# Optimization experiments

Hardware: AMD Instinct MI355X
Metric: run time of the kernel (lower is better)

## Reference

```python
import jax, jax.numpy as jnp
import numpy as np

NUM_CAPS = 10        # num_output_capsules
OUT_CH = 16          # output_cap_channels (output capsule dim)
IN_CH = 256
H = W = 6
PRIM_DIM = 8
NUM_PRIM = OUT_CH * H * W // PRIM_DIM  # 72 primary capsule vectors per branch
NUM_ITERS = 3
EPS = 1e-8


def squash(s, axis=-1):
    # v = (|s|^2 / (1 + |s|^2)) * s / |s|
    sq = jnp.sum(s * s, axis=axis, keepdims=True)
    return (sq / (1.0 + sq)) * s * jax.lax.rsqrt(sq + EPS)


def setup_inputs() -> dict:
    key = jax.random.key(0)
    k1, k2, k3, k4 = jax.random.split(key, 4)
    B = 2048
    x = jax.random.normal(k1, (B, IN_CH, H, W), dtype=jnp.float32)
    # per-output-capsule 1x1 conv: weight [K, out_ch, in_ch], bias [K, out_ch]
    conv_w = jax.random.normal(k2, (NUM_CAPS, OUT_CH, IN_CH), dtype=jnp.float32) * (1.0 / np.sqrt(IN_CH))
    conv_b = jnp.zeros((NUM_CAPS, OUT_CH), dtype=jnp.float32)
    # transformation matrices: [K, P, prim_dim, out_dim]
    weights = jax.random.normal(k3, (NUM_CAPS, NUM_PRIM, PRIM_DIM, OUT_CH), dtype=jnp.float32)
    return {"x": x, "conv_w": conv_w, "conv_b": conv_b, "weights": weights}


def reference(x, conv_w, conv_b, weights):
    B = x.shape[0]
    # 1x1 conv per output capsule branch: [B, K, out_ch, H, W]
    caps = jnp.einsum('bchw,koc->bkohw', x, conv_w) + conv_b[None, :, :, None, None]
    # flatten + reshape into primary capsule vectors: [B, K, P, 8]
    prim = caps.reshape(B, NUM_CAPS, NUM_PRIM, PRIM_DIM)
    # prediction vectors u = prim @ W : [B, K, P, 16]
    u = jnp.einsum('bkpd,kpde->bkpe', prim, weights)
    # dynamic routing by agreement
    b = jnp.zeros((B, NUM_CAPS, NUM_PRIM), dtype=u.dtype)
    v = None
    for _ in range(NUM_ITERS):
        c = jax.nn.softmax(b, axis=1)                 # coupling over output capsules
        s = jnp.einsum('bkp,bkpe->bke', c, u)         # weighted sum over primaries
        v = squash(s, axis=-1)                        # [B, K, 16]
        b = b + jnp.einsum('bkpe,bke->bkp', u, v)     # agreement
    return v
```

## Files before the change

### kernel.cpp

```cpp
#include <hip/hip_runtime.h>
#include <stdint.h>

#define KCAPS 10
#define OC    16
#define IC    256
#define HWSZ  36
#define PRIM  72
#define PD    8
#define EDIM  16
#define BMAX  2048

typedef short bf16x8 __attribute__((ext_vector_type(8)));
typedef float f32x4  __attribute__((ext_vector_type(4)));

__device__ unsigned short g_whi[KCAPS * OC * IC];
__device__ unsigned short g_wlo[KCAPS * OC * IC];
__device__ float4         g_wtsT4[KCAPS * PD * 4 * PRIM];
__device__ float          g_caps_fallback[(size_t)BMAX * 160 * HWSZ];

#define SMEM_G 76032
#define SMEM_B (13194 * 4)

__device__ __forceinline__ void bf_split(float v, unsigned short& hb, unsigned short& lb) {
    __bf16 h = (__bf16)v;
    hb = __builtin_bit_cast(unsigned short, h);
    __bf16 l = (__bf16)(v - (float)h);
    lb = __builtin_bit_cast(unsigned short, l);
}

__device__ __forceinline__ f32x4 mfma16(bf16x8 a, bf16x8 b, f32x4 c) {
    return __builtin_amdgcn_mfma_f32_16x16x32_bf16(a, b, c, 0, 0, 0);
}

__global__ __launch_bounds__(256)
void prep_kernel(const float* __restrict__ w, const float* __restrict__ wts) {
    int i = blockIdx.x * 256 + threadIdx.x;
    if (i < KCAPS * OC * IC) {
        unsigned short hb, lb;
        bf_split(w[i], hb, lb);
        g_whi[i] = hb;
        g_wlo[i] = lb;
    }
    if (i < KCAPS * PD * 4 * PRIM) {
        int p = i % PRIM;
        int r = i / PRIM;
        int e4 = r & 3;
        int d  = (r >> 2) & 7;
        int k  = r >> 5;
        g_wtsT4[i] = *(const float4*)(wts + (size_t)(((k * PRIM + p) * PD + d) * EDIM + e4 * 4));
    }
}

__global__ __launch_bounds__(256, 2)
void gemm_caps(const float* __restrict__ x, const float* __restrict__ conv_b,
               float* __restrict__ caps_g) {
    extern __shared__ char smem[];
    uint32_t* xs_u = (uint32_t*)smem;
    const short* xs_s = (const short*)smem;

    const int t  = threadIdx.x;
    const int bb = blockIdx.x;
    const int wv = t >> 6;
    const int ln = t & 63;
    const int row = ln & 15;
    const int g   = ln >> 4;
    const int nm  = (wv < 2) ? 3 : 2;

    for (int task = t; task < 2304; task += 256) {
        int half = (task >= 1152) ? 1 : 0;
        int tt = task - half * 1152;
        int cp = tt / 9, hq = tt - cp * 9;
        const float4* x4 = (const float4*)(x + (size_t)(2 * bb + half) * (IC * HWSZ));
        float4 va = x4[(2 * cp) * 9 + hq];
        float4 vb = x4[(2 * cp + 1) * 9 + hq];
        uint32_t* xh = xs_u + half * 9504;
        uint32_t* xl = xh + 4752;
        int base = (4 * hq) * 132 + cp;
        unsigned short ha, la, hb, lb;
        bf_split(va.x, ha, la); bf_split(vb.x, hb, lb);
        xh[base]       = (uint32_t)ha | ((uint32_t)hb << 16);
        xl[base]       = (uint32_t)la | ((uint32_t)lb << 16);
        bf_split(va.y, ha, la); bf_split(vb.y, hb, lb);
        xh[base + 132] = (uint32_t)ha | ((uint32_t)hb << 16);
        xl[base + 132] = (uint32_t)la | ((uint32_t)lb << 16);
        bf_split(va.z, ha, la); bf_split(vb.z, hb, lb);
        xh[base + 264] = (uint32_t)ha | ((uint32_t)hb << 16);
        xl[base + 264] = (uint32_t)la | ((uint32_t)lb << 16);
        bf_split(va.w, ha, la); bf_split(vb.w, hb, lb);
        xh[base + 396] = (uint32_t)ha | ((uint32_t)hb << 16);
        xl[base + 396] = (uint32_t)la | ((uint32_t)lb << 16);
    }
    __syncthreads();

    const int hwbase[3] = {0, 16, 20};

    f32x4 acc0[3][3] = {}, acc1[3][3] = {};
    for (int kt = 0; kt < 8; ++kt) {
        bf16x8 bh[3], bl[3];
        #pragma unroll
        for (int mi = 0; mi < 3; ++mi) {
            if (mi < nm) {
                int woff = ((wv + 4 * mi) * 16 + row) * 256 + kt * 32 + g * 8;
                bh[mi] = *(const bf16x8*)(g_whi + woff);
                bl[mi] = *(const bf16x8*)(g_wlo + woff);
            }
        }
        bf16x8 ah0[3], al0[3], ah1[3], al1[3];
        #pragma unroll
        for (int nt = 0; nt < 3; ++nt) {
            int o2 = (hwbase[nt] + row) * 264 + kt * 32 + g * 8;
            ah0[nt] = *(const bf16x8*)(xs_s + o2);
            al0[nt] = *(const bf16x8*)(xs_s + 9504 + o2);
            ah1[nt] = *(const bf16x8*)(xs_s + 19008 + o2);
            al1[nt] = *(const bf16x8*)(xs_s + 28512 + o2);
        }
        #pragma unroll
        for (int mi = 0; mi < 3; ++mi) {
            if (mi < nm) {
                #pragma unroll
                for (int nt = 0; nt < 3; ++nt) {
                    acc0[mi][nt] = mfma16(ah0[nt], bh[mi], acc0[mi][nt]);
                    acc1[mi][nt] = mfma16(ah1[nt], bh[mi], acc1[mi][nt]);
                    acc0[mi][nt] = mfma16(al0[nt], bh[mi], acc0[mi][nt]);
                    acc1[mi][nt] = mfma16(al1[nt], bh[mi], acc1[mi][nt]);
                    acc0[mi][nt] = mfma16(ah0[nt], bl[mi], acc0[mi][nt]);
                    acc1[mi][nt] = mfma16(ah1[nt], bl[mi], acc1[mi][nt]);
                }
            }
        }
    }

    float* cg0 = caps_g + (size_t)(2 * bb) * (160 * HWSZ);
    float* cg1 = caps_g + (size_t)(2 * bb + 1) * (160 * HWSZ);
    #pragma unroll
    for (int mi = 0; mi < 3; ++mi) {
        if (mi < nm) {
            int m = (wv + 4 * mi) * 16 + row;
            float bias = conv_b[m];
            #pragma unroll
            for (int nt = 0; nt < 3; ++nt) {
                int hw0 = hwbase[nt] + g * 4;
                if (nt < 2 || g == 3) {
                    float4 o0, o1;
                    o0.x = acc0[mi][nt][0] + bias; o1.x = acc1[mi][nt][0] + bias;
                    o0.y = acc0[mi][nt][1] + bias; o1.y = acc1[mi][nt][1] + bias;
                    o0.z = acc0[mi][nt][2] + bias; o1.z = acc1[mi][nt][2] + bias;
                    o0.w = acc0[mi][nt][3] + bias; o1.w = acc1[mi][nt][3] + bias;
                    *(float4*)(cg0 + m * HWSZ + hw0) = o0;
                    *(float4*)(cg1 + m * HWSZ + hw0) = o1;
                }
            }
        }
    }
}

__global__ __launch_bounds__(256, 2)
void route_kernel(const float* __restrict__ caps_g, float* __restrict__ out) {
    extern __shared__ char smem[];
    float* u_t     = (float*)smem;
    float* b_s     = u_t + 16 * 724;
    float* c_s     = b_s + 720;
    float* v_s     = c_s + 720;
    float* scale_s = v_s + 160;

    const int t  = threadIdx.x;
    const int bb = blockIdx.x;

    {
        const float4* cg4 = (const float4*)(caps_g + (size_t)bb * (160 * HWSZ));
        for (int task = t; task < KCAPS * PRIM; task += 256) {
            int k = task / PRIM;
            int p = task - k * PRIM;
            float4 c0 = cg4[task * 2];
            float4 c1 = cg4[task * 2 + 1];
            float pv[PD] = {c0.x, c0.y, c0.z, c0.w, c1.x, c1.y, c1.z, c1.w};
            const float4* wb = g_wtsT4 + k * (PD * 4 * PRIM) + p;
            float au[EDIM] = {};
            #pragma unroll
            for (int d = 0; d < PD; ++d) {
                #pragma unroll
                for (int e4 = 0; e4 < 4; ++e4) {
                    float4 w4 = wb[(d * 4 + e4) * PRIM];
                    au[e4 * 4 + 0] = fmaf(pv[d], w4.x, au[e4 * 4 + 0]);
                    au[e4 * 4 + 1] = fmaf(pv[d], w4.y, au[e4 * 4 + 1]);
                    au[e4 * 4 + 2] = fmaf(pv[d], w4.z, au[e4 * 4 + 2]);
                    au[e4 * 4 + 3] = fmaf(pv[d], w4.w, au[e4 * 4 + 3]);
                }
            }
            #pragma unroll
            for (int e = 0; e < EDIM; ++e) u_t[e * 724 + task] = au[e];
        }
    }
    for (int i = t; i < KCAPS * PRIM; i += 256) b_s[i] = 0.f;
    __syncthreads();

    for (int it = 0; it < 3; ++it) {
        if (t < PRIM) {
            float bv[KCAPS];
            float m = -1e30f;
            #pragma unroll
            for (int k2 = 0; k2 < KCAPS; ++k2) { bv[k2] = b_s[k2 * PRIM + t]; m = fmaxf(m, bv[k2]); }
            float sum = 0.f;
            #pragma unroll
            for (int k2 = 0; k2 < KCAPS; ++k2) { bv[k2] = __expf(bv[k2] - m); sum += bv[k2]; }
            float inv = 1.f / sum;
            #pragma unroll
            for (int k2 = 0; k2 < KCAPS; ++k2) c_s[k2 * PRIM + t] = bv[k2] * inv;
        }
        __syncthreads();

        if (t < KCAPS * EDIM) {
            int k = t >> 4, e = t & 15;
            float s = 0.f;
            const float* ur = u_t + e * 724 + k * PRIM;
            const float* cr = c_s + k * PRIM;
            for (int p = 0; p < PRIM; ++p) s = fmaf(cr[p], ur[p], s);
            v_s[t] = s;
        }
        __syncthreads();

        if (t < KCAPS) {
            float sq = 0.f;
            #pragma unroll
            for (int e = 0; e < EDIM; ++e) { float sv = v_s[t * EDIM + e]; sq = fmaf(sv, sv, sq); }
            scale_s[t] = (sq / (1.f + sq)) * rsqrtf(sq + 1e-8f);
        }
        __syncthreads();

        if (t < KCAPS * EDIM) v_s[t] *= scale_s[t >> 4];
        __syncthreads();

        if (it < 2) {
            for (int task = t; task < KCAPS * PRIM; task += 256) {
                int k = task / PRIM;
                float dot = 0.f;
                const float* vr = v_s + k * EDIM;
                #pragma unroll
                for (int e = 0; e < EDIM; ++e) dot = fmaf(u_t[e * 724 + task], vr[e], dot);
                b_s[task] += dot;
            }
            __syncthreads();
        }
    }

    if (t < KCAPS * EDIM) out[(size_t)bb * (KCAPS * EDIM) + t] = v_s[t];
}

extern "C" void kernel_launch(void* const* d_in, const int* in_sizes, int n_in,
                              void* d_out, int out_size, void* d_ws, size_t ws_size,
                              hipStream_t stream) {
    const float* x  = (const float*)d_in[0];
    const float* cw = (const float*)d_in[1];
    const float* cb = (const float*)d_in[2];
    const float* wt = (const float*)d_in[3];
    float* out = (float*)d_out;
    const int B = in_sizes[0] / (IC * HWSZ);

    size_t capsNeed = (size_t)B * 160 * HWSZ * sizeof(float);
    float* caps_g = nullptr;
    if (d_ws != nullptr && ws_size >= capsNeed) {
        caps_g = (float*)d_ws;
    } else {
        void* sym = nullptr;
        hipGetSymbolAddress(&sym, HIP_SYMBOL(g_caps_fallback));
        caps_g = (float*)sym;
    }

    hipLaunchKernelGGL(prep_kernel, dim3(160), dim3(256), 0, stream, cw, wt);

    hipFuncSetAttribute(reinterpret_cast<const void*>(&gemm_caps),
                        hipFuncAttributeMaxDynamicSharedMemorySize, SMEM_G);
    hipLaunchKernelGGL(gemm_caps, dim3(B / 2), dim3(256), SMEM_G, stream, x, cb, caps_g);

    hipFuncSetAttribute(reinterpret_cast<const void*>(&route_kernel),
                        hipFuncAttributeMaxDynamicSharedMemorySize, SMEM_B);
    hipLaunchKernelGGL(route_kernel, dim3(B), dim3(256), SMEM_B, stream, caps_g, out);
}
```

Before: 95.39 us.

## Restructure routing kernel: fuse squash via shuffles, specialize first iteration, widen block

Changes the routing kernel in several ways. The first iteration is special-cased to a uniform mean, since softmax of zero logits is 0.1, which skips the softmax and the b zero-init. Squash is computed with wave shuffles inside the weighted-sum step instead of in separate stages, which removes two barriers per iteration. The weighted-sum loops are vectorised to float4, and the block grows to 512 threads so the u-projection and agreement loops cover all 720 tasks in one pass. A larger block may reduce how many blocks fit per CU.

```diff
diff --git a/kernel.cpp b/kernel.cpp
--- a/kernel.cpp
+++ b/kernel.cpp
@@ -19,7 +19,7 @@
 __device__ float          g_caps_fallback[(size_t)BMAX * 160 * HWSZ];
 
 #define SMEM_G 76032
-#define SMEM_B (13194 * 4)
+#define SMEM_R (13184 * 4)
 
 __device__ __forceinline__ void bf_split(float v, unsigned short& hb, unsigned short& lb) {
     __bf16 h = (__bf16)v;
@@ -154,21 +154,20 @@
     }
 }
 
-__global__ __launch_bounds__(256, 2)
+__global__ __launch_bounds__(512, 2)
 void route_kernel(const float* __restrict__ caps_g, float* __restrict__ out) {
     extern __shared__ char smem[];
-    float* u_t     = (float*)smem;
-    float* b_s     = u_t + 16 * 724;
-    float* c_s     = b_s + 720;
-    float* v_s     = c_s + 720;
-    float* scale_s = v_s + 160;
+    float* u_t = (float*)smem;
+    float* b_s = u_t + 16 * 724;
+    float* c_s = b_s + 720;
+    float* v_s = c_s + 720;
 
     const int t  = threadIdx.x;
     const int bb = blockIdx.x;
 
     {
         const float4* cg4 = (const float4*)(caps_g + (size_t)bb * (160 * HWSZ));
-        for (int task = t; task < KCAPS * PRIM; task += 256) {
+        for (int task = t; task < KCAPS * PRIM; task += 512) {
             int k = task / PRIM;
             int p = task - k * PRIM;
             float4 c0 = cg4[task * 2];
@@ -191,10 +190,38 @@
             for (int e = 0; e < EDIM; ++e) u_t[e * 724 + task] = au[e];
         }
     }
-    for (int i = t; i < KCAPS * PRIM; i += 256) b_s[i] = 0.f;
     __syncthreads();
 
-    for (int it = 0; it < 3; ++it) {
+    if (t < KCAPS * EDIM) {
+        int k = t >> 4, e = t & 15;
+        const float4* ur4 = (const float4*)(u_t + e * 724 + k * PRIM);
+        float s = 0.f;
+        #pragma unroll
+        for (int j = 0; j < 18; ++j) {
+            float4 u4 = ur4[j];
+            s += (u4.x + u4.y) + (u4.z + u4.w);
+        }
+        s *= 0.1f;
+        float q = s * s;
+        q += __shfl_xor(q, 1); q += __shfl_xor(q, 2);
+        q += __shfl_xor(q, 4); q += __shfl_xor(q, 8);
+        v_s[t] = s * (q / (1.f + q)) * rsqrtf(q + 1e-8f);
+    }
+    __syncthreads();
+
+    for (int task = t; task < KCAPS * PRIM; task += 512) {
+        int k = task / PRIM;
+        const float* vr = v_s + k * EDIM;
+        float dot = 0.f;
+        #pragma unroll
+        for (int e = 0; e < EDIM; ++e) dot = fmaf(u_t[e * 724 + task], vr[e], dot);
+        b_s[task] = dot;
+    }
+    __syncthreads();
+
+    float vout = 0.f;
+    #pragma unroll
+    for (int it = 1; it < 3; ++it) {
         if (t < PRIM) {
             float bv[KCAPS];
             float m = -1e30f;
@@ -211,30 +238,32 @@
 
         if (t < KCAPS * EDIM) {
             int k = t >> 4, e = t & 15;
+            const float4* ur4 = (const float4*)(u_t + e * 724 + k * PRIM);
+            const float4* cr4 = (const float4*)(c_s + k * PRIM);
             float s = 0.f;
-            const float* ur = u_t + e * 724 + k * PRIM;
-            const float* cr = c_s + k * PRIM;
-            for (int p = 0; p < PRIM; ++p) s = fmaf(cr[p], ur[p], s);
-            v_s[t] = s;
+            #pragma unroll
+            for (int j = 0; j < 18; ++j) {
+                float4 u4 = ur4[j];
+                float4 c4 = cr4[j];
+                s = fmaf(u4.x, c4.x, s);
+                s = fmaf(u4.y, c4.y, s);
+                s = fmaf(u4.z, c4.z, s);
+                s = fmaf(u4.w, c4.w, s);
+            }
+            float q = s * s;
+            q += __shfl_xor(q, 1); q += __shfl_xor(q, 2);
+            q += __shfl_xor(q, 4); q += __shfl_xor(q, 8);
+            float v = s * (q / (1.f + q)) * rsqrtf(q + 1e-8f);
+            if (it < 2) v_s[t] = v;
+            else vout = v;
         }
         __syncthreads();
 
-        if (t < KCAPS) {
-            float sq = 0.f;
-            #pragma unroll
-            for (int e = 0; e < EDIM; ++e) { float sv = v_s[t * EDIM + e]; sq = fmaf(sv, sv, sq); }
-            scale_s[t] = (sq / (1.f + sq)) * rsqrtf(sq + 1e-8f);
-        }
-        __syncthreads();
-
-        if (t < KCAPS * EDIM) v_s[t] *= scale_s[t >> 4];
-        __syncthreads();
-
         if (it < 2) {
-            for (int task = t; task < KCAPS * PRIM; task += 256) {
+            for (int task = t; task < KCAPS * PRIM; task += 512) {
                 int k = task / PRIM;
+                const float* vr = v_s + k * EDIM;
                 float dot = 0.f;
-                const float* vr = v_s + k * EDIM;
                 #pragma unroll
                 for (int e = 0; e < EDIM; ++e) dot = fmaf(u_t[e * 724 + task], vr[e], dot);
                 b_s[task] += dot;
@@ -243,7 +272,7 @@
         }
     }
 
-    if (t < KCAPS * EDIM) out[(size_t)bb * (KCAPS * EDIM) + t] = v_s[t];
+    if (t < KCAPS * EDIM) out[(size_t)bb * (KCAPS * EDIM) + t] = vout;
 }
 
 extern "C" void kernel_launch(void* const* d_in, const int* in_sizes, int n_in,
@@ -273,6 +302,6 @@
     hipLaunchKernelGGL(gemm_caps, dim3(B / 2), dim3(256), SMEM_G, stream, x, cb, caps_g);
 
     hipFuncSetAttribute(reinterpret_cast<const void*>(&route_kernel),
-                        hipFuncAttributeMaxDynamicSharedMemorySize, SMEM_B);
-    hipLaunchKernelGGL(route_kernel, dim3(B), dim3(256), SMEM_B, stream, caps_g, out);
-}
+                        hipFuncAttributeMaxDynamicSharedMemorySize, SMEM_R);
+    hipLaunchKernelGGL(route_kernel, dim3(B), dim3(512), SMEM_R, stream, caps_g, out);
+}
```

Result: faster. 85.31 us (-10.6%).
